# Optimization experiments

Measured on AMD Instinct MI355X. Metric: run time of the kernel, lower is better.

The kernel has to match this reference:

```python
import jax, jax.numpy as jnp
import numpy as np

SUB = 40   # subframe_size
NSUB = 4   # nb_subframes


def _glu(x, w):
    return x * jax.nn.sigmoid(x @ w.T)


def _gru(x, h, w_ih, w_hh):
    # torch.nn.GRUCell (bias=False): gates ordered r, z, n
    H = h.shape[-1]
    gi = x @ w_ih.T
    gh = h @ w_hh.T
    r = jax.nn.sigmoid(gi[:, :H] + gh[:, :H])
    z = jax.nn.sigmoid(gi[:, H:2 * H] + gh[:, H:2 * H])
    n = jnp.tanh(gi[:, 2 * H:] + r * gh[:, 2 * H:])
    return (1.0 - z) * n + z * h


def _fargan_forward(features, period, p):
    B, T, _ = features.shape
    period = jnp.clip(period, 32, 254)

    # ---- FARGANCond ----
    f = features[:, 2:, :]                               # [B, T-2, 20]
    pidx = jnp.clip(period[:, 2:] - 32, 0, 223)
    pe = p['pembed'][pidx]                               # [B, T-2, 12]
    x = jnp.tanh(jnp.concatenate([f, pe], -1) @ p['fd1_w'].T)   # [B, T-2, 64]
    y = jax.lax.conv_general_dilated(
        x.transpose(0, 2, 1), p['fconv1_w'], (1,), 'VALID',
        dimension_numbers=('NCH', 'OIH', 'NCH'))
    y = jnp.tanh(y).transpose(0, 2, 1)                   # [B, T-4, 128]
    cond = jnp.tanh(y @ p['fd2_w'].T)                    # [B, T-4, 320]

    nb_frames = T - 4
    cond_steps = cond.reshape(B, nb_frames, NSUB, 80)
    cond_steps = cond_steps.transpose(1, 2, 0, 3).reshape(nb_frames * NSUB, B, 80)
    pitch = period[:, 3:3 + nb_frames]                   # conv-center aligned pitch
    pitch_steps = jnp.repeat(pitch.T, NSUB, axis=0)      # [steps, B]

    rng = jnp.arange(SUB + 4)

    def step(carry, inp):
        exc_mem, prev_pred, s1, s2, s3, fwc_state = carry
        cond80, per = inp
        gain = 0.2 + 0.8 * jax.nn.sigmoid(cond80 @ p['cg_w'].T + p['cg_b'])
        gain = jnp.clip(gain, 0.001, 20.0)               # [B, 1]
        idx = 256 - per[:, None] + rng[None, :] - 2
        idx = idx - (idx >= 256) * per[:, None]
        idx = jnp.clip(idx, 0, 255)
        pred = jnp.take_along_axis(exc_mem, idx, axis=1) / (1e-5 + gain)  # [B, 44]
        prev = exc_mem[:, -SUB:] / (1e-5 + gain)         # [B, 40]
        tmp = jnp.concatenate([cond80, pred, prev], 1)   # [B, 164]
        fpitch = pred[:, 2:-2]                           # [B, 40]
        xcat = jnp.concatenate([fwc_state, tmp], 1)      # [B, 328]
        fwc_out = _glu(jnp.tanh(xcat @ p['fwc_w'].T), p['fwc_glu_w'])  # [B, 192]
        new_fwc_state = xcat[:, 164:]
        pg = jax.nn.sigmoid(fwc_out @ p['gout_w'].T + p['gout_b'])     # [B, 4]
        s1n = _gru(jnp.concatenate([fwc_out, pg[:, 0:1] * fpitch, prev], 1), s1, p['g1_ih'], p['g1_hh'])
        g1 = _glu(s1n, p['glu1_w'])
        s2n = _gru(jnp.concatenate([g1, pg[:, 1:2] * fpitch, prev], 1), s2, p['g2_ih'], p['g2_hh'])
        g2 = _glu(s2n, p['glu2_w'])
        s3n = _gru(jnp.concatenate([g2, pg[:, 2:3] * fpitch, prev], 1), s3, p['g3_ih'], p['g3_hh'])
        g3 = _glu(s3n, p['glu3_w'])
        skip_in = jnp.concatenate([g1, g2, g3, fwc_out, pg[:, 3:4] * fpitch, prev], 1)  # [B, 688+80]
        skip = _glu(jnp.tanh(skip_in @ p['skip_w'].T), p['skip_glu_w'])
        sig = jnp.tanh(skip @ p['sig_w'].T) * gain       # [B, 40]
        exc_mem = jnp.concatenate([exc_mem[:, SUB:], sig], 1)
        prev_pred = jnp.concatenate([prev_pred[:, SUB:], fpitch], 1)
        return (exc_mem, prev_pred, s1n, s2n, s3n, new_fwc_state), sig

    dt = features.dtype
    carry0 = (jnp.zeros((B, 256), dt), jnp.zeros((B, 256), dt),
              jnp.zeros((B, 160), dt), jnp.zeros((B, 128), dt),
              jnp.zeros((B, 128), dt), jnp.zeros((B, 164), dt))
    _, sigs = jax.lax.scan(jax.checkpoint(step), carry0, (cond_steps, pitch_steps))
    return sigs.transpose(1, 0, 2).reshape(B, -1)        # [B, nb_frames*160]


def _w(key, out_dim, in_dim):
    return jax.random.normal(key, (out_dim, in_dim), jnp.float32) / np.sqrt(in_dim)


def setup_inputs() -> dict:
    key = jax.random.key(0)
    ks = jax.random.split(key, 24)
    B, T = 128, 504
    d = {}
    d['features'] = jax.random.normal(ks[0], (B, T, 20), jnp.float32)
    d['period'] = jax.random.randint(ks[1], (B, T), 32, 255)
    d['pembed'] = jax.random.normal(ks[2], (224, 12), jnp.float32) * 0.3
    d['fd1_w'] = _w(ks[3], 64, 32)
    d['fconv1_w'] = jax.random.normal(ks[4], (128, 64, 3), jnp.float32) / np.sqrt(192.0)
    d['fd2_w'] = _w(ks[5], 320, 128)
    d['cg_w'] = _w(ks[6], 1, 80)
    d['cg_b'] = jnp.zeros((1,), jnp.float32)
    d['fwc_w'] = _w(ks[7], 192, 328)
    d['fwc_glu_w'] = _w(ks[8], 192, 192)
    d['g1_ih'] = _w(ks[9], 480, 272)
    d['g1_hh'] = _w(ks[10], 480, 160)
    d['glu1_w'] = _w(ks[11], 160, 160)
    d['g2_ih'] = _w(ks[12], 384, 240)
    d['g2_hh'] = _w(ks[13], 384, 128)
    d['glu2_w'] = _w(ks[14], 128, 128)
    d['g3_ih'] = _w(ks[15], 384, 208)
    d['g3_hh'] = _w(ks[16], 384, 128)
    d['glu3_w'] = _w(ks[17], 128, 128)
    d['skip_w'] = _w(ks[18], 128, 688)
    d['skip_glu_w'] = _w(ks[19], 128, 128)
    d['sig_w'] = _w(ks[20], 40, 128)
    d['gout_w'] = _w(ks[21], 4, 192)
    d['gout_b'] = jnp.zeros((4,), jnp.float32)
    return d


def reference(features, period, pembed, fd1_w, fconv1_w, fd2_w, cg_w, cg_b,
              fwc_w, fwc_glu_w, g1_ih, g1_hh, glu1_w, g2_ih, g2_hh, glu2_w,
              g3_ih, g3_hh, glu3_w, skip_w, skip_glu_w, sig_w, gout_w, gout_b):
    p = dict(pembed=pembed, fd1_w=fd1_w, fconv1_w=fconv1_w, fd2_w=fd2_w,
             cg_w=cg_w, cg_b=cg_b, fwc_w=fwc_w, fwc_glu_w=fwc_glu_w,
             g1_ih=g1_ih, g1_hh=g1_hh, glu1_w=glu1_w,
             g2_ih=g2_ih, g2_hh=g2_hh, glu2_w=glu2_w,
             g3_ih=g3_ih, g3_hh=g3_hh, glu3_w=glu3_w,
             skip_w=skip_w, skip_glu_w=skip_glu_w, sig_w=sig_w,
             gout_w=gout_w, gout_b=gout_b)
    return _fargan_forward(features, period, p)
```

## Files before the change

kernel.cpp:

```cpp
#include <hip/hip_runtime.h>
#include <hip/hip_fp16.h>
#include <math.h>


#define DEV __device__ __forceinline__

DEV float sigm(float x) { return 1.0f / (1.0f + __expf(-x)); }
DEV float tanh_f(float x) { return 1.0f - 2.0f / (__expf(2.0f * x) + 1.0f); }

typedef _Float16 h2v __attribute__((ext_vector_type(2)));

#if defined(__has_builtin)
#if __has_builtin(__builtin_amdgcn_fdot2)
#define HAVE_FDOT2 1
#endif
#endif

DEV float fdot2(h2v a, h2v b, float c) {
#ifdef HAVE_FDOT2
    return __builtin_amdgcn_fdot2(a, b, c, false);
#else
    return c + (float)a[0] * (float)b[0] + (float)a[1] * (float)b[1];
#endif
}

constexpr size_t STEPS = 2000;
constexpr size_t OFF_X     = 0;
constexpr size_t OFF_Y     = 4200000;
constexpr size_t OFF_GAIN  = 12392000;
constexpr size_t OFF_CONDH = 12648000;
constexpr size_t OFF_W     = 22888000;

constexpr size_t W_FWC     = 0;
constexpr size_t W_FWCGLU  = W_FWC    + 192*352;
constexpr size_t W_GOUT    = W_FWCGLU + 192*192;
constexpr size_t W_G1IH    = W_GOUT   + 4*192;
constexpr size_t W_G1HH    = W_G1IH   + 480*272;
constexpr size_t W_GLU1    = W_G1HH   + 480*160;
constexpr size_t W_G2IH    = W_GLU1   + 160*160;
constexpr size_t W_G2HH    = W_G2IH   + 384*240;
constexpr size_t W_GLU2    = W_G2HH   + 384*128;
constexpr size_t W_G3IH    = W_GLU2   + 128*128;
constexpr size_t W_G3HH    = W_G3IH   + 384*208;
constexpr size_t W_GLU3    = W_G3HH   + 384*128;
constexpr size_t W_SKIP    = W_GLU3   + 128*128;
constexpr size_t W_SKIPGLU = W_SKIP   + 128*704;
constexpr size_t W_SIG     = W_SKIPGLU+ 128*128;

constexpr int WL_FWCGLU = 0;
constexpr int WL_GLU2   = 4608;
constexpr int WL_GLU3   = 6656;
constexpr int WL_TOT    = 8704;

__global__ void k_pack_h(const float* __restrict__ src, __half* __restrict__ dst,
                         int OUT, int K, int KP8) {
    int t = blockIdx.x * 256 + threadIdx.x;
    if (t >= OUT * KP8) return;
    int j = t % OUT;
    int k8 = t / OUT;
    __half* d = dst + (size_t)t * 8;
#pragma unroll
    for (int i = 0; i < 8; ++i) {
        int k = k8 * 8 + i;
        d[i] = (k < K) ? __float2half(src[(size_t)j * K + k]) : __float2half(0.0f);
    }
}

__global__ void k_feat(const float* __restrict__ features, const int* __restrict__ period,
                       const float* __restrict__ pembed, const float* __restrict__ fd1,
                       float* __restrict__ xbuf) {
    int t = blockIdx.x * 256 + threadIdx.x;
    const int total = 128 * 502 * 64;
    if (t >= total) return;
    int o = t & 63;
    int r = t >> 6;
    int ft = r % 502;
    int b = r / 502;
    const float* f = features + ((size_t)b * 504 + ft + 2) * 20;
    int per = period[b * 504 + ft + 2];
    per = min(max(per, 32), 254);
    const float* pe = pembed + (per - 32) * 12;
    const float* w = fd1 + o * 32;
    float acc = 0.0f;
#pragma unroll
    for (int i = 0; i < 20; ++i) acc += f[i] * w[i];
#pragma unroll
    for (int i = 0; i < 12; ++i) acc += pe[i] * w[20 + i];
    xbuf[t] = tanh_f(acc);
}

__global__ void k_conv(const float* __restrict__ xbuf, const float* __restrict__ fconv1,
                       float* __restrict__ ybuf) {
    int t = blockIdx.x * 256 + threadIdx.x;
    const int total = 128 * 500 * 128;
    if (t >= total) return;
    int oc = t & 127;
    int r = t >> 7;
    int tt = r % 500;
    int b = r / 500;
    const float* xp = xbuf + ((size_t)b * 502 + tt) * 64;
    const float* w = fconv1 + oc * 192;
    float acc = 0.0f;
#pragma unroll 8
    for (int i = 0; i < 64; ++i) {
        acc += xp[i] * w[i * 3 + 0];
        acc += xp[64 + i] * w[i * 3 + 1];
        acc += xp[128 + i] * w[i * 3 + 2];
    }
    ybuf[t] = tanh_f(acc);
}

__global__ void k_cond(const float* __restrict__ ybuf, const float* __restrict__ fd2,
                       __half* __restrict__ cond) {
    int b = blockIdx.x / 50;
    int t0 = (blockIdx.x % 50) * 10;
    int tid = threadIdx.x;
    __shared__ float yl[1280];
    for (int i = tid; i < 1280; i += 320)
        yl[i] = ybuf[((size_t)b * 500 + t0) * 128 + i];
    __syncthreads();
    const float* w = fd2 + tid * 128;
    float acc[10];
#pragma unroll
    for (int q = 0; q < 10; ++q) acc[q] = 0.0f;
#pragma unroll 4
    for (int k = 0; k < 128; ++k) {
        float wv = w[k];
#pragma unroll
        for (int q = 0; q < 10; ++q) acc[q] += wv * yl[q * 128 + k];
    }
#pragma unroll
    for (int q = 0; q < 10; ++q)
        cond[((size_t)b * 500 + t0 + q) * 320 + tid] = __float2half(tanh_f(acc[q]));
}

__global__ void k_gain(const __half* __restrict__ cond, const float* __restrict__ cgw,
                       const float* __restrict__ cgb, float* __restrict__ gains) {
    int t = blockIdx.x * 256 + threadIdx.x;
    const int total = 128 * 2000;
    if (t >= total) return;
    int s = t % 2000;
    int b = t / 2000;
    int frame = s >> 2, sub = s & 3;
    const __half* c = cond + ((size_t)b * 500 + frame) * 320 + sub * 80;
    float acc = 0.0f;
#pragma unroll 8
    for (int i = 0; i < 80; ++i) acc += __half2float(c[i]) * cgw[i];
    float g = 0.2f + 0.8f * sigm(acc + cgb[0]);
    g = fminf(20.0f, fmaxf(0.001f, g));
    gains[t] = g;
}

DEV void dot8h(uint4 w, uint4 x, float& a0, float& a1) {
    const h2v* wv = (const h2v*)&w;
    const h2v* xv = (const h2v*)&x;
    a0 = fdot2(wv[0], xv[0], a0);
    a1 = fdot2(wv[1], xv[1], a1);
    a0 = fdot2(wv[2], xv[2], a0);
    a1 = fdot2(wv[3], xv[3], a1);
}

template <int OUT, int KP8, int S>
DEV void mv_partial(const uint4* __restrict__ WT, const __half* __restrict__ x,
                    float* __restrict__ part, int tid) {
    static_assert(KP8 % S == 0, "KP8 % S");
    static_assert(OUT * S <= 1024, "threads");
    constexpr int KS8 = KP8 / S;
    if (tid < OUT * S) {
        int j = tid % OUT;
        int sl = tid / OUT;
        const uint4* w = WT + (size_t)sl * KS8 * OUT + j;
        const uint4* xx = (const uint4*)x + (size_t)sl * KS8;
        float a0 = 0.0f, a1 = 0.0f;
#pragma unroll 4
        for (int k = 0; k < KS8; ++k) dot8h(w[(size_t)k * OUT], xx[k], a0, a1);
        part[tid] = a0 + a1;
    }
}

template <int OUT, int KP8, int S>
DEV void mv_partial_l(const uint4* wl, const __half* __restrict__ x,
                      float* __restrict__ part, int tid) {
    constexpr int KS8 = KP8 / S;
    if (tid < OUT * S) {
        int j = tid % OUT;
        int sl = tid / OUT;
        const uint4* w = wl + (size_t)sl * KS8 * OUT + j;
        const uint4* xx = (const uint4*)x + (size_t)sl * KS8;
        float a0 = 0.0f, a1 = 0.0f;
#pragma unroll
        for (int k = 0; k < KS8; ++k) dot8h(w[(size_t)k * OUT], xx[k], a0, a1);
        part[tid] = a0 + a1;
    }
}

template <int OUT, int KP8A, int KP8B>
DEV void gru_partial(const uint4* __restrict__ wa, const __half* __restrict__ xa,
                     const uint4* __restrict__ wb, const __half* __restrict__ xb,
                     float* __restrict__ pa, float* __restrict__ pb, int tid) {
    static_assert((KP8A % 2 == 0) && (KP8B % 2 == 0), "even");
    constexpr int KA = KP8A / 2, KB = KP8B / 2;
    if (tid < OUT * 2) {
        int j = tid % OUT;
        int sl = tid / OUT;
        {
            const uint4* w = wa + (size_t)sl * KA * OUT + j;
            const uint4* xx = (const uint4*)xa + (size_t)sl * KA;
            float a0 = 0.0f, a1 = 0.0f;
#pragma unroll 4
            for (int k = 0; k < KA; ++k) dot8h(w[(size_t)k * OUT], xx[k], a0, a1);
            pa[tid] = a0 + a1;
        }
        {
            const uint4* w = wb + (size_t)sl * KB * OUT + j;
            const uint4* xx = (const uint4*)xb + (size_t)sl * KB;
            float b0 = 0.0f, b1 = 0.0f;
#pragma unroll 4
            for (int k = 0; k < KB; ++k) dot8h(w[(size_t)k * OUT], xx[k], b0, b1);
            pb[tid] = b0 + b1;
        }
    }
}

template <int H>
DEV void gru_update(const float* __restrict__ pa, const float* __restrict__ pb,
                    float* __restrict__ s, __half* __restrict__ sh, int tid) {
    constexpr int OUT = 3 * H;
    if (tid < H) {
        float gi_r = pa[tid] + pa[OUT + tid];
        float gh_r = pb[tid] + pb[OUT + tid];
        float gi_z = pa[H + tid] + pa[OUT + H + tid];
        float gh_z = pb[H + tid] + pb[OUT + H + tid];
        float gi_n = pa[2 * H + tid] + pa[OUT + 2 * H + tid];
        float gh_n = pb[2 * H + tid] + pb[OUT + 2 * H + tid];
        float r = sigm(gi_r + gh_r);
        float z = sigm(gi_z + gh_z);
        float n = tanh_f(gi_n + r * gh_n);
        float v = (1.0f - z) * n + z * s[tid];
        s[tid] = v;
        sh[tid] = __float2half(v);
    }
}

__global__ __launch_bounds__(1024) void fargan_main(const float* __restrict__ ws,
                                                    const int* __restrict__ period,
                                                    const float* __restrict__ goutb,
                                                    float* __restrict__ out) {
    const int b = blockIdx.x;
    const int tid = threadIdx.x;

    const __half* cond = (const __half*)(ws + OFF_CONDH);
    const float* gains = ws + OFF_GAIN;
    const __half* whb  = (const __half*)(ws + OFF_W);
    const uint4* wFWC     = (const uint4*)(whb + W_FWC);
    const uint4* wFWCGLU  = (const uint4*)(whb + W_FWCGLU);
    const uint4* wGOUT    = (const uint4*)(whb + W_GOUT);
    const uint4* wG1IH    = (const uint4*)(whb + W_G1IH);
    const uint4* wG1HH    = (const uint4*)(whb + W_G1HH);
    const uint4* wGLU1    = (const uint4*)(whb + W_GLU1);
    const uint4* wG2IH    = (const uint4*)(whb + W_G2IH);
    const uint4* wG2HH    = (const uint4*)(whb + W_G2HH);
    const uint4* wGLU2    = (const uint4*)(whb + W_GLU2);
    const uint4* wG3IH    = (const uint4*)(whb + W_G3IH);
    const uint4* wG3HH    = (const uint4*)(whb + W_G3HH);
    const uint4* wGLU3    = (const uint4*)(whb + W_GLU3);
    const uint4* wSKIP    = (const uint4*)(whb + W_SKIP);
    const uint4* wSKIPGLU = (const uint4*)(whb + W_SKIPGLU);
    const uint4* wSIG     = (const uint4*)(whb + W_SIG);

    __shared__ __align__(16) uint4 wlds[WL_TOT];

    __shared__ __align__(16) __half xcat_h[352];
    __shared__ __align__(16) __half inb_h[272];
    __shared__ __align__(16) __half fwcpre_h[192], fwcout_h[192];
    __shared__ __align__(16) __half s1_h[160], s2_h[128], s3_h[128];
    __shared__ __align__(16) __half g1_h[160], g2_h[128], g3_h[128];
    __shared__ __align__(16) __half skipin_h[704], skippre_h[128], skipout_h[128];
    __shared__ __align__(16) float exc[256];
    __shared__ __align__(16) float s1[160], s2[128], s3[128];
    __shared__ __align__(16) float partA[1024], partB[1024];
    __shared__ __align__(16) float fwcpre[192];
    __shared__ __align__(16) float pg[4];
    __shared__ __align__(16) float skippre[128];
    __shared__ __align__(16) float sigraw[40];

    for (int i = tid; i < 4608; i += 1024) wlds[WL_FWCGLU + i] = wFWCGLU[i];
    for (int i = tid; i < 2048; i += 1024) wlds[WL_GLU2 + i] = wGLU2[i];
    for (int i = tid; i < 2048; i += 1024) wlds[WL_GLU3 + i] = wGLU3[i];

    const int j2 = tid % 384;
    const int sl2 = (tid < 768) ? (tid / 384) : 0;
    const uint4* g2b = wG2HH + (size_t)sl2 * 8 * 384 + j2;
    const uint4 c0 = g2b[0 * 384];
    const uint4 c1 = g2b[1 * 384];
    const uint4 c2 = g2b[2 * 384];
    const uint4 c3 = g2b[3 * 384];
    const uint4 c4 = g2b[4 * 384];
    const uint4 c5 = g2b[5 * 384];
    const uint4 c6 = g2b[6 * 384];
    const uint4 c7 = g2b[7 * 384];

    for (int i = tid; i < 256; i += 1024) exc[i] = 0.0f;
    if (tid < 160) { s1[tid] = 0.0f; s1_h[tid] = __float2half(0.0f); }
    if (tid < 128) { s2[tid] = 0.0f; s3[tid] = 0.0f;
                     s2_h[tid] = __float2half(0.0f); s3_h[tid] = __float2half(0.0f); }
    if (tid < 164) xcat_h[tid] = __float2half(0.0f);
    if (tid >= 328 && tid < 352) xcat_h[tid] = __float2half(0.0f);
    if (tid >= 688 && tid < 704) skipin_h[tid] = __float2half(0.0f);
    __syncthreads();

    for (int s = 0; s < (int)STEPS; ++s) {
        const int frame = s >> 2;
        const float gain = gains[(size_t)b * 2000 + s];
        const float ig = 1.0f / (1e-5f + gain);
        int per = period[b * 504 + 3 + frame];
        per = min(max(per, 32), 254);

        if (tid < 80) {
            xcat_h[164 + tid] = cond[((size_t)b * 500 + frame) * 320 + (s & 3) * 80 + tid];
        } else if (tid >= 128 && tid < 172) {
            int j = tid - 128;
            int idx = 254 - per + j;
            if (idx >= 256) idx -= per;
            idx = min(255, max(0, idx));
            xcat_h[244 + j] = __float2half(exc[idx] * ig);
        } else if (tid >= 192 && tid < 232) {
            xcat_h[288 + tid - 192] = __float2half(exc[216 + tid - 192] * ig);
        }
        __syncthreads();

        mv_partial<192, 44, 4>(wFWC, xcat_h, partA, tid);
        __syncthreads();
        if (tid < 192) {
            float a = partA[tid] + partA[192 + tid] + partA[384 + tid] + partA[576 + tid];
            float t = tanh_f(a);
            fwcpre[tid] = t;
            fwcpre_h[tid] = __float2half(t);
        }
        __syncthreads();

        mv_partial_l<192, 24, 4>(wlds + WL_FWCGLU, fwcpre_h, partA, tid);
        if (tid >= 768 && tid < 800) {
            int t2 = tid - 768;
            int j = t2 & 3, sl = t2 >> 2;
            const uint4* w = wGOUT + (sl * 3) * 4 + j;
            const uint4* xx = (const uint4*)fwcpre_h + sl * 3;
            float a0 = 0.0f, a1 = 0.0f;
#pragma unroll
            for (int k = 0; k < 3; ++k) dot8h(w[k * 4], xx[k], a0, a1);
            partB[t2] = a0 + a1;
        } else if (tid >= 832 && tid < 996) {
            xcat_h[tid - 832] = xcat_h[tid - 832 + 164];
        }
        __syncthreads();

        if (tid < 192) {
            float a = partA[tid] + partA[192 + tid] + partA[384 + tid] + partA[576 + tid];
            float v = fwcpre[tid] * sigm(a);
            __half vh = __float2half(v);
            fwcout_h[tid] = vh;
            inb_h[tid] = vh;
        } else if (tid < 232) {
            float a = goutb[0];
#pragma unroll
            for (int sl = 0; sl < 8; ++sl) a += partB[sl * 4];
            inb_h[tid] = __float2half(sigm(a) * __half2float(xcat_h[246 + tid - 192]));
        } else if (tid < 272) {
            inb_h[tid] = xcat_h[288 + tid - 232];
        } else if (tid >= 960 && tid < 964) {
            int j = tid - 960;
            float a = goutb[j];
#pragma unroll
            for (int sl = 0; sl < 8; ++sl) a += partB[sl * 4 + j];
            pg[j] = sigm(a);
        }
        __syncthreads();

        gru_partial<480, 34, 20>(wG1IH, inb_h, wG1HH, s1_h, partA, partB, tid);
        __syncthreads();
        gru_update<160>(partA, partB, s1, s1_h, tid);
        __syncthreads();

        mv_partial<160, 20, 4>(wGLU1, s1_h, partA, tid);
        __syncthreads();
        if (tid < 160) {
            float a = partA[tid] + partA[160 + tid] + partA[320 + tid] + partA[480 + tid];
            float v = s1[tid] * sigm(a);
            __half vh = __float2half(v);
            g1_h[tid] = vh;
            inb_h[tid] = vh;
        } else if (tid < 200) {
            inb_h[tid] = __float2half(pg[1] * __half2float(xcat_h[246 + tid - 160]));
        } else if (tid < 240) {
            inb_h[tid] = xcat_h[288 + tid - 200];
        }
        __syncthreads();

        if (tid < 768) {
            constexpr int KA = 15;
            {
                const uint4* w = wG2IH + (size_t)sl2 * KA * 384 + j2;
                const uint4* xx = (const uint4*)inb_h + (size_t)sl2 * KA;
                float a0 = 0.0f, a1 = 0.0f;
#pragma unroll 4
                for (int k = 0; k < KA; ++k) dot8h(w[(size_t)k * 384], xx[k], a0, a1);
                partA[tid] = a0 + a1;
            }
            {
                const uint4* xb = (const uint4*)s2_h + (size_t)sl2 * 8;
                float b0 = 0.0f, b1 = 0.0f;
                dot8h(c0, xb[0], b0, b1);
                dot8h(c1, xb[1], b0, b1);
                dot8h(c2, xb[2], b0, b1);
                dot8h(c3, xb[3], b0, b1);
                dot8h(c4, xb[4], b0, b1);
                dot8h(c5, xb[5], b0, b1);
                dot8h(c6, xb[6], b0, b1);
                dot8h(c7, xb[7], b0, b1);
                partB[tid] = b0 + b1;
            }
        }
        __syncthreads();
        gru_update<128>(partA, partB, s2, s2_h, tid);
        __syncthreads();

        mv_partial_l<128, 16, 8>(wlds + WL_GLU2, s2_h, partA, tid);
        __syncthreads();
        if (tid < 128) {
            float a = 0.0f;
#pragma unroll
            for (int sl = 0; sl < 8; ++sl) a += partA[sl * 128 + tid];
            float v = s2[tid] * sigm(a);
            __half vh = __float2half(v);
            g2_h[tid] = vh;
            inb_h[tid] = vh;
        } else if (tid < 168) {
            inb_h[tid] = __float2half(pg[2] * __half2float(xcat_h[246 + tid - 128]));
        } else if (tid < 208) {
            inb_h[tid] = xcat_h[288 + tid - 168];
        }
        __syncthreads();

        gru_partial<384, 26, 16>(wG3IH, inb_h, wG3HH, s3_h, partA, partB, tid);
        __syncthreads();
        gru_update<128>(partA, partB, s3, s3_h, tid);
        __syncthreads();

        mv_partial_l<128, 16, 8>(wlds + WL_GLU3, s3_h, partA, tid);
        __syncthreads();
        if (tid < 128) {
            float a = 0.0f;
#pragma unroll
            for (int sl = 0; sl < 8; ++sl) a += partA[sl * 128 + tid];
            float v = s3[tid] * sigm(a);
            __half vh = __float2half(v);
            g3_h[tid] = vh;
            skipin_h[288 + tid] = vh;
        } else if (tid < 288) {
            skipin_h[tid - 128] = g1_h[tid - 128];
        } else if (tid < 416) {
            skipin_h[160 + tid - 288] = g2_h[tid - 288];
        } else if (tid < 608) {
            skipin_h[tid] = fwcout_h[tid - 416];
        } else if (tid < 648) {
            skipin_h[tid] = __float2half(pg[3] * __half2float(xcat_h[246 + tid - 608]));
        } else if (tid < 688) {
            skipin_h[tid] = xcat_h[288 + tid - 648];
        }
        __syncthreads();

        mv_partial<128, 88, 8>(wSKIP, skipin_h, partA, tid);
        __syncthreads();
        if (tid < 128) {
            float a = 0.0f;
#pragma unroll
            for (int sl = 0; sl < 8; ++sl) a += partA[sl * 128 + tid];
            float t = tanh_f(a);
            skippre[tid] = t;
            skippre_h[tid] = __float2half(t);
        }
        __syncthreads();

        mv_partial<128, 16, 8>(wSKIPGLU, skippre_h, partA, tid);
        __syncthreads();
        if (tid < 128) {
            float a = 0.0f;
#pragma unroll
            for (int sl = 0; sl < 8; ++sl) a += partA[sl * 128 + tid];
            skipout_h[tid] = __float2half(skippre[tid] * sigm(a));
        }
        __syncthreads();

        mv_partial<40, 16, 8>(wSIG, skipout_h, partA, tid);
        __syncthreads();
        float keep = (tid < 216) ? exc[tid + 40] : 0.0f;
        if (tid < 40) {
            float a = 0.0f;
#pragma unroll
            for (int sl = 0; sl < 8; ++sl) a += partA[sl * 40 + tid];
            sigraw[tid] = tanh_f(a) * gain;
        }
        __syncthreads();
        if (tid < 216) {
            exc[tid] = keep;
        } else if (tid < 256) {
            float sv = sigraw[tid - 216];
            exc[tid] = sv;
            out[(size_t)b * 80000 + (size_t)s * 40 + (tid - 216)] = sv;
        }
        __syncthreads();
    }
}

extern "C" void kernel_launch(void* const* d_in, const int* in_sizes, int n_in,
                              void* d_out, int out_size, void* d_ws, size_t ws_size,
                              hipStream_t stream) {
    const float* features = (const float*)d_in[0];
    const int*   period   = (const int*)d_in[1];
    const float* pembed   = (const float*)d_in[2];
    const float* fd1_w    = (const float*)d_in[3];
    const float* fconv1_w = (const float*)d_in[4];
    const float* fd2_w    = (const float*)d_in[5];
    const float* cg_w     = (const float*)d_in[6];
    const float* cg_b     = (const float*)d_in[7];
    const float* fwc_w    = (const float*)d_in[8];
    const float* fwc_glu  = (const float*)d_in[9];
    const float* g1_ih    = (const float*)d_in[10];
    const float* g1_hh    = (const float*)d_in[11];
    const float* glu1_w   = (const float*)d_in[12];
    const float* g2_ih    = (const float*)d_in[13];
    const float* g2_hh    = (const float*)d_in[14];
    const float* glu2_w   = (const float*)d_in[15];
    const float* g3_ih    = (const float*)d_in[16];
    const float* g3_hh    = (const float*)d_in[17];
    const float* glu3_w   = (const float*)d_in[18];
    const float* skip_w   = (const float*)d_in[19];
    const float* skip_glu = (const float*)d_in[20];
    const float* sig_w    = (const float*)d_in[21];
    const float* gout_w   = (const float*)d_in[22];
    const float* gout_b   = (const float*)d_in[23];

    float* ws = (float*)d_ws;
    float* out = (float*)d_out;
    __half* wh = (__half*)(ws + OFF_W);

    struct PW { const float* src; size_t off; int out, k, kpad; };
    const PW pws[15] = {
        {fwc_w,    W_FWC,     192, 328, 352}, {fwc_glu, W_FWCGLU, 192, 192, 192},
        {gout_w,   W_GOUT,      4, 192, 192}, {g1_ih,   W_G1IH,   480, 272, 272},
        {g1_hh,    W_G1HH,    480, 160, 160}, {glu1_w,  W_GLU1,   160, 160, 160},
        {g2_ih,    W_G2IH,    384, 240, 240}, {g2_hh,   W_G2HH,   384, 128, 128},
        {glu2_w,   W_GLU2,    128, 128, 128}, {g3_ih,   W_G3IH,   384, 208, 208},
        {g3_hh,    W_G3HH,    384, 128, 128}, {glu3_w,  W_GLU3,   128, 128, 128},
        {skip_w,   W_SKIP,    128, 688, 704}, {skip_glu,W_SKIPGLU,128, 128, 128},
        {sig_w,    W_SIG,      40, 128, 128},
    };
    for (int i = 0; i < 15; ++i) {
        int kp8 = pws[i].kpad / 8;
        int n = pws[i].out * kp8;
        k_pack_h<<<(n + 255) / 256, 256, 0, stream>>>(pws[i].src, wh + pws[i].off,
                                                      pws[i].out, pws[i].k, kp8);
    }

    {
        int n = 128 * 502 * 64;
        k_feat<<<(n + 255) / 256, 256, 0, stream>>>(features, period, pembed, fd1_w,
                                                    ws + OFF_X);
    }
    {
        int n = 128 * 500 * 128;
        k_conv<<<(n + 255) / 256, 256, 0, stream>>>(ws + OFF_X, fconv1_w, ws + OFF_Y);
    }
    k_cond<<<128 * 50, 320, 0, stream>>>(ws + OFF_Y, fd2_w, (__half*)(ws + OFF_CONDH));
    {
        int n = 128 * 2000;
        k_gain<<<(n + 255) / 256, 256, 0, stream>>>((const __half*)(ws + OFF_CONDH),
                                                    cg_w, cg_b, ws + OFF_GAIN);
    }

    fargan_main<<<128, 1024, 0, stream>>>(ws, period, gout_b, out);
}
```

Before: 34.19 ms.

## Process two batch elements per block to reuse each weight load

```diff
diff --git a/kernel.cpp b/kernel.cpp
--- a/kernel.cpp
+++ b/kernel.cpp
@@ -49,8 +49,9 @@
 
 constexpr int WL_FWCGLU = 0;
 constexpr int WL_GLU2   = 4608;
-constexpr int WL_GLU3   = 6656;
-constexpr int WL_TOT    = 8704;
+constexpr int WL_SIG    = 6656;
+constexpr int WL_GOUT   = 7296;
+constexpr int WL_TOT    = 7392;
 
 __global__ void k_pack_h(const float* __restrict__ src, __half* __restrict__ dst,
                          int OUT, int K, int KP8) {
@@ -151,53 +152,64 @@
     gains[t] = g;
 }
 
-DEV void dot8h(uint4 w, uint4 x, float& a0, float& a1) {
+DEV void dot8h2(uint4 w, uint4 x0, uint4 x1,
+                float& a0, float& a1, float& b0, float& b1) {
     const h2v* wv = (const h2v*)&w;
-    const h2v* xv = (const h2v*)&x;
-    a0 = fdot2(wv[0], xv[0], a0);
-    a1 = fdot2(wv[1], xv[1], a1);
-    a0 = fdot2(wv[2], xv[2], a0);
-    a1 = fdot2(wv[3], xv[3], a1);
+    const h2v* x0v = (const h2v*)&x0;
+    const h2v* x1v = (const h2v*)&x1;
+    a0 = fdot2(wv[0], x0v[0], a0);
+    b0 = fdot2(wv[0], x1v[0], b0);
+    a1 = fdot2(wv[1], x0v[1], a1);
+    b1 = fdot2(wv[1], x1v[1], b1);
+    a0 = fdot2(wv[2], x0v[2], a0);
+    b0 = fdot2(wv[2], x1v[2], b0);
+    a1 = fdot2(wv[3], x0v[3], a1);
+    b1 = fdot2(wv[3], x1v[3], b1);
 }
 
 template <int OUT, int KP8, int S>
-DEV void mv_partial(const uint4* __restrict__ WT, const __half* __restrict__ x,
-                    float* __restrict__ part, int tid) {
+DEV void mv2(const uint4* __restrict__ WT, const __half* x0, const __half* x1,
+             float* p0, float* p1, int tid) {
     static_assert(KP8 % S == 0, "KP8 % S");
-    static_assert(OUT * S <= 1024, "threads");
     constexpr int KS8 = KP8 / S;
     if (tid < OUT * S) {
         int j = tid % OUT;
         int sl = tid / OUT;
         const uint4* w = WT + (size_t)sl * KS8 * OUT + j;
-        const uint4* xx = (const uint4*)x + (size_t)sl * KS8;
-        float a0 = 0.0f, a1 = 0.0f;
+        const uint4* xx0 = (const uint4*)x0 + (size_t)sl * KS8;
+        const uint4* xx1 = (const uint4*)x1 + (size_t)sl * KS8;
+        float a0 = 0.0f, a1 = 0.0f, b0 = 0.0f, b1 = 0.0f;
 #pragma unroll 4
-        for (int k = 0; k < KS8; ++k) dot8h(w[(size_t)k * OUT], xx[k], a0, a1);
-        part[tid] = a0 + a1;
+        for (int k = 0; k < KS8; ++k)
+            dot8h2(w[(size_t)k * OUT], xx0[k], xx1[k], a0, a1, b0, b1);
+        p0[tid] = a0 + a1;
+        p1[tid] = b0 + b1;
     }
 }
 
 template <int OUT, int KP8, int S>
-DEV void mv_partial_l(const uint4* wl, const __half* __restrict__ x,
-                      float* __restrict__ part, int tid) {
+DEV void mv2_l(const uint4* wl, const __half* x0, const __half* x1,
+               float* p0, float* p1, int tid) {
     constexpr int KS8 = KP8 / S;
     if (tid < OUT * S) {
         int j = tid % OUT;
         int sl = tid / OUT;
         const uint4* w = wl + (size_t)sl * KS8 * OUT + j;
-        const uint4* xx = (const uint4*)x + (size_t)sl * KS8;
-        float a0 = 0.0f, a1 = 0.0f;
-#pragma unroll
-        for (int k = 0; k < KS8; ++k) dot8h(w[(size_t)k * OUT], xx[k], a0, a1);
-        part[tid] = a0 + a1;
+        const uint4* xx0 = (const uint4*)x0 + (size_t)sl * KS8;
+        const uint4* xx1 = (const uint4*)x1 + (size_t)sl * KS8;
+        float a0 = 0.0f, a1 = 0.0f, b0 = 0.0f, b1 = 0.0f;
+#pragma unroll
+        for (int k = 0; k < KS8; ++k)
+            dot8h2(w[(size_t)k * OUT], xx0[k], xx1[k], a0, a1, b0, b1);
+        p0[tid] = a0 + a1;
+        p1[tid] = b0 + b1;
     }
 }
 
 template <int OUT, int KP8A, int KP8B>
-DEV void gru_partial(const uint4* __restrict__ wa, const __half* __restrict__ xa,
-                     const uint4* __restrict__ wb, const __half* __restrict__ xb,
-                     float* __restrict__ pa, float* __restrict__ pb, int tid) {
+DEV void gru_p2(const uint4* __restrict__ wa, const __half* xa0, const __half* xa1,
+                const uint4* __restrict__ wb, const __half* xb0, const __half* xb1,
+                float* pa0, float* pa1, float* pb0, float* pb1, int tid) {
     static_assert((KP8A % 2 == 0) && (KP8B % 2 == 0), "even");
     constexpr int KA = KP8A / 2, KB = KP8B / 2;
     if (tid < OUT * 2) {
@@ -205,19 +217,25 @@
         int sl = tid / OUT;
         {
             const uint4* w = wa + (size_t)sl * KA * OUT + j;
-            const uint4* xx = (const uint4*)xa + (size_t)sl * KA;
-            float a0 = 0.0f, a1 = 0.0f;
+            const uint4* x0 = (const uint4*)xa0 + (size_t)sl * KA;
+            const uint4* x1 = (const uint4*)xa1 + (size_t)sl * KA;
+            float a0 = 0.0f, a1 = 0.0f, b0 = 0.0f, b1 = 0.0f;
 #pragma unroll 4
-            for (int k = 0; k < KA; ++k) dot8h(w[(size_t)k * OUT], xx[k], a0, a1);
-            pa[tid] = a0 + a1;
+            for (int k = 0; k < KA; ++k)
+                dot8h2(w[(size_t)k * OUT], x0[k], x1[k], a0, a1, b0, b1);
+            pa0[tid] = a0 + a1;
+            pa1[tid] = b0 + b1;
         }
         {
             const uint4* w = wb + (size_t)sl * KB * OUT + j;
-            const uint4* xx = (const uint4*)xb + (size_t)sl * KB;
-            float b0 = 0.0f, b1 = 0.0f;
+            const uint4* x0 = (const uint4*)xb0 + (size_t)sl * KB;
+            const uint4* x1 = (const uint4*)xb1 + (size_t)sl * KB;
+            float a0 = 0.0f, a1 = 0.0f, b0 = 0.0f, b1 = 0.0f;
 #pragma unroll 4
-            for (int k = 0; k < KB; ++k) dot8h(w[(size_t)k * OUT], xx[k], b0, b1);
-            pb[tid] = b0 + b1;
+            for (int k = 0; k < KB; ++k)
+                dot8h2(w[(size_t)k * OUT], x0[k], x1[k], a0, a1, b0, b1);
+            pb0[tid] = a0 + a1;
+            pb1[tid] = b0 + b1;
         }
     }
 }
@@ -246,7 +264,8 @@
                                                     const int* __restrict__ period,
                                                     const float* __restrict__ goutb,
                                                     float* __restrict__ out) {
-    const int b = blockIdx.x;
+    const int bid = blockIdx.x;
+    const int b0 = 2 * bid, b1 = 2 * bid + 1;
     const int tid = threadIdx.x;
 
     const __half* cond = (const __half*)(ws + OFF_CONDH);
@@ -270,243 +289,296 @@
 
     __shared__ __align__(16) uint4 wlds[WL_TOT];
 
-    __shared__ __align__(16) __half xcat_h[352];
-    __shared__ __align__(16) __half inb_h[272];
-    __shared__ __align__(16) __half fwcpre_h[192], fwcout_h[192];
-    __shared__ __align__(16) __half s1_h[160], s2_h[128], s3_h[128];
-    __shared__ __align__(16) __half g1_h[160], g2_h[128], g3_h[128];
-    __shared__ __align__(16) __half skipin_h[704], skippre_h[128], skipout_h[128];
-    __shared__ __align__(16) float exc[256];
-    __shared__ __align__(16) float s1[160], s2[128], s3[128];
-    __shared__ __align__(16) float partA[1024], partB[1024];
-    __shared__ __align__(16) float fwcpre[192];
-    __shared__ __align__(16) float pg[4];
-    __shared__ __align__(16) float skippre[128];
-    __shared__ __align__(16) float sigraw[40];
-
-    for (int i = tid; i < 4608; i += 1024) wlds[WL_FWCGLU + i] = wFWCGLU[i];
-    for (int i = tid; i < 2048; i += 1024) wlds[WL_GLU2 + i] = wGLU2[i];
-    for (int i = tid; i < 2048; i += 1024) wlds[WL_GLU3 + i] = wGLU3[i];
-
-    const int j2 = tid % 384;
-    const int sl2 = (tid < 768) ? (tid / 384) : 0;
-    const uint4* g2b = wG2HH + (size_t)sl2 * 8 * 384 + j2;
-    const uint4 c0 = g2b[0 * 384];
-    const uint4 c1 = g2b[1 * 384];
-    const uint4 c2 = g2b[2 * 384];
-    const uint4 c3 = g2b[3 * 384];
-    const uint4 c4 = g2b[4 * 384];
-    const uint4 c5 = g2b[5 * 384];
-    const uint4 c6 = g2b[6 * 384];
-    const uint4 c7 = g2b[7 * 384];
-
-    for (int i = tid; i < 256; i += 1024) exc[i] = 0.0f;
-    if (tid < 160) { s1[tid] = 0.0f; s1_h[tid] = __float2half(0.0f); }
-    if (tid < 128) { s2[tid] = 0.0f; s3[tid] = 0.0f;
-                     s2_h[tid] = __float2half(0.0f); s3_h[tid] = __float2half(0.0f); }
-    if (tid < 164) xcat_h[tid] = __float2half(0.0f);
-    if (tid >= 328 && tid < 352) xcat_h[tid] = __float2half(0.0f);
-    if (tid >= 688 && tid < 704) skipin_h[tid] = __float2half(0.0f);
+    __shared__ __align__(16) __half xcat_h[2][352];
+    __shared__ __align__(16) __half inb_h[2][272];
+    __shared__ __align__(16) __half fwcpre_h[2][192], fwcout_h[2][192];
+    __shared__ __align__(16) __half s1_h[2][160], s2_h[2][128], s3_h[2][128];
+    __shared__ __align__(16) __half g1_h[2][160], g2_h[2][128], g3_h[2][128];
+    __shared__ __align__(16) __half skipin_h[2][704], skippre_h[2][128], skipout_h[2][128];
+    __shared__ __align__(16) float exc[2][256];
+    __shared__ __align__(16) float s1[2][160], s2[2][128], s3[2][128];
+    __shared__ __align__(16) float partA[2][1024], partB[2][1024];
+    __shared__ __align__(16) float fwcpre[2][192];
+    __shared__ __align__(16) float pg[2][4];
+    __shared__ __align__(16) float skippre[2][128];
+    __shared__ __align__(16) float sigraw[2][40];
+
+    for (int i = tid; i < WL_TOT; i += 1024) {
+        uint4 v;
+        if (i < 4608)      v = wFWCGLU[i];
+        else if (i < 6656) v = wGLU2[i - 4608];
+        else if (i < 7296) v = wSIG[i - 6656];
+        else               v = wGOUT[i - 7296];
+        wlds[i] = v;
+    }
+
+    for (int i = tid; i < 512; i += 1024) ((float*)exc)[i] = 0.0f;
+    if (tid < 160) {
+        s1[0][tid] = 0.0f; s1[1][tid] = 0.0f;
+        s1_h[0][tid] = __float2half(0.0f); s1_h[1][tid] = __float2half(0.0f);
+    }
+    if (tid < 128) {
+        s2[0][tid] = 0.0f; s2[1][tid] = 0.0f;
+        s3[0][tid] = 0.0f; s3[1][tid] = 0.0f;
+        s2_h[0][tid] = __float2half(0.0f); s2_h[1][tid] = __float2half(0.0f);
+        s3_h[0][tid] = __float2half(0.0f); s3_h[1][tid] = __float2half(0.0f);
+    }
+    if (tid < 164) {
+        xcat_h[0][tid] = __float2half(0.0f);
+        xcat_h[1][tid] = __float2half(0.0f);
+    }
+    if (tid >= 328 && tid < 352) {
+        xcat_h[0][tid] = __float2half(0.0f);
+        xcat_h[1][tid] = __float2half(0.0f);
+    }
+    if (tid >= 688 && tid < 704) {
+        skipin_h[0][tid] = __float2half(0.0f);
+        skipin_h[1][tid] = __float2half(0.0f);
+    }
     __syncthreads();
 
     for (int s = 0; s < (int)STEPS; ++s) {
         const int frame = s >> 2;
-        const float gain = gains[(size_t)b * 2000 + s];
-        const float ig = 1.0f / (1e-5f + gain);
-        int per = period[b * 504 + 3 + frame];
-        per = min(max(per, 32), 254);
+        const float gn0 = gains[(size_t)b0 * 2000 + s];
+        const float gn1 = gains[(size_t)b1 * 2000 + s];
+        const float ig0 = 1.0f / (1e-5f + gn0);
+        const float ig1 = 1.0f / (1e-5f + gn1);
+        int per0 = min(max(period[b0 * 504 + 3 + frame], 32), 254);
+        int per1 = min(max(period[b1 * 504 + 3 + frame], 32), 254);
 
         if (tid < 80) {
-            xcat_h[164 + tid] = cond[((size_t)b * 500 + frame) * 320 + (s & 3) * 80 + tid];
+            xcat_h[0][164 + tid] = cond[((size_t)b0 * 500 + frame) * 320 + (s & 3) * 80 + tid];
+            xcat_h[1][164 + tid] = cond[((size_t)b1 * 500 + frame) * 320 + (s & 3) * 80 + tid];
         } else if (tid >= 128 && tid < 172) {
             int j = tid - 128;
-            int idx = 254 - per + j;
-            if (idx >= 256) idx -= per;
-            idx = min(255, max(0, idx));
-            xcat_h[244 + j] = __float2half(exc[idx] * ig);
+            {
+                int idx = 254 - per0 + j;
+                if (idx >= 256) idx -= per0;
+                idx = min(255, max(0, idx));
+                xcat_h[0][244 + j] = __float2half(exc[0][idx] * ig0);
+            }
+            {
+                int idx = 254 - per1 + j;
+                if (idx >= 256) idx -= per1;
+                idx = min(255, max(0, idx));
+                xcat_h[1][244 + j] = __float2half(exc[1][idx] * ig1);
+            }
         } else if (tid >= 192 && tid < 232) {
-            xcat_h[288 + tid - 192] = __float2half(exc[216 + tid - 192] * ig);
-        }
-        __syncthreads();
-
-        mv_partial<192, 44, 4>(wFWC, xcat_h, partA, tid);
+            int j = tid - 192;
+            xcat_h[0][288 + j] = __float2half(exc[0][216 + j] * ig0);
+            xcat_h[1][288 + j] = __float2half(exc[1][216 + j] * ig1);
+        }
+        __syncthreads();
+
+        mv2<192, 44, 4>(wFWC, xcat_h[0], xcat_h[1], partA[0], partA[1], tid);
         __syncthreads();
         if (tid < 192) {
-            float a = partA[tid] + partA[192 + tid] + partA[384 + tid] + partA[576 + tid];
-            float t = tanh_f(a);
-            fwcpre[tid] = t;
-            fwcpre_h[tid] = __float2half(t);
-        }
-        __syncthreads();
-
-        mv_partial_l<192, 24, 4>(wlds + WL_FWCGLU, fwcpre_h, partA, tid);
+#pragma unroll
+            for (int g = 0; g < 2; ++g) {
+                float a = partA[g][tid] + partA[g][192 + tid] + partA[g][384 + tid] + partA[g][576 + tid];
+                float t = tanh_f(a);
+                fwcpre[g][tid] = t;
+                fwcpre_h[g][tid] = __float2half(t);
+            }
+        }
+        __syncthreads();
+
+        mv2_l<192, 24, 4>(wlds + WL_FWCGLU, fwcpre_h[0], fwcpre_h[1], partA[0], partA[1], tid);
         if (tid >= 768 && tid < 800) {
             int t2 = tid - 768;
             int j = t2 & 3, sl = t2 >> 2;
-            const uint4* w = wGOUT + (sl * 3) * 4 + j;
-            const uint4* xx = (const uint4*)fwcpre_h + sl * 3;
-            float a0 = 0.0f, a1 = 0.0f;
-#pragma unroll
-            for (int k = 0; k < 3; ++k) dot8h(w[k * 4], xx[k], a0, a1);
-            partB[t2] = a0 + a1;
+            const uint4* w = wlds + WL_GOUT + (sl * 3) * 4 + j;
+            const uint4* xx0 = (const uint4*)fwcpre_h[0] + sl * 3;
+            const uint4* xx1 = (const uint4*)fwcpre_h[1] + sl * 3;
+            float a0 = 0.0f, a1 = 0.0f, c0 = 0.0f, c1 = 0.0f;
+#pragma unroll
+            for (int k = 0; k < 3; ++k) dot8h2(w[k * 4], xx0[k], xx1[k], a0, a1, c0, c1);
+            partB[0][t2] = a0 + a1;
+            partB[1][t2] = c0 + c1;
         } else if (tid >= 832 && tid < 996) {
-            xcat_h[tid - 832] = xcat_h[tid - 832 + 164];
+            xcat_h[0][tid - 832] = xcat_h[0][tid - 832 + 164];
+            xcat_h[1][tid - 832] = xcat_h[1][tid - 832 + 164];
         }
         __syncthreads();
 
         if (tid < 192) {
-            float a = partA[tid] + partA[192 + tid] + partA[384 + tid] + partA[576 + tid];
-            float v = fwcpre[tid] * sigm(a);
-            __half vh = __float2half(v);
-            fwcout_h[tid] = vh;
-            inb_h[tid] = vh;
+#pragma unroll
+            for (int g = 0; g < 2; ++g) {
+                float a = partA[g][tid] + partA[g][192 + tid] + partA[g][384 + tid] + partA[g][576 + tid];
+                float v = fwcpre[g][tid] * sigm(a);
+                __half vh = __float2half(v);
+                fwcout_h[g][tid] = vh;
+                inb_h[g][tid] = vh;
+            }
         } else if (tid < 232) {
-            float a = goutb[0];
-#pragma unroll
-            for (int sl = 0; sl < 8; ++sl) a += partB[sl * 4];
-            inb_h[tid] = __float2half(sigm(a) * __half2float(xcat_h[246 + tid - 192]));
+#pragma unroll
+            for (int g = 0; g < 2; ++g) {
+                float a = goutb[0];
+#pragma unroll
+                for (int sl = 0; sl < 8; ++sl) a += partB[g][sl * 4];
+                inb_h[g][tid] = __float2half(sigm(a) * __half2float(xcat_h[g][246 + tid - 192]));
+            }
         } else if (tid < 272) {
-            inb_h[tid] = xcat_h[288 + tid - 232];
+            inb_h[0][tid] = xcat_h[0][288 + tid - 232];
+            inb_h[1][tid] = xcat_h[1][288 + tid - 232];
         } else if (tid >= 960 && tid < 964) {
             int j = tid - 960;
-            float a = goutb[j];
-#pragma unroll
-            for (int sl = 0; sl < 8; ++sl) a += partB[sl * 4 + j];
-            pg[j] = sigm(a);
-        }
-        __syncthreads();
-
-        gru_partial<480, 34, 20>(wG1IH, inb_h, wG1HH, s1_h, partA, partB, tid);
-        __syncthreads();
-        gru_update<160>(partA, partB, s1, s1_h, tid);
-        __syncthreads();
-
-        mv_partial<160, 20, 4>(wGLU1, s1_h, partA, tid);
+#pragma unroll
+            for (int g = 0; g < 2; ++g) {
+                float a = goutb[j];
+#pragma unroll
+                for (int sl = 0; sl < 8; ++sl) a += partB[g][sl * 4 + j];
+                pg[g][j] = sigm(a);
+            }
+        }
+        __syncthreads();
+
+        gru_p2<480, 34, 20>(wG1IH, inb_h[0], inb_h[1], wG1HH, s1_h[0], s1_h[1],
+                            partA[0], partA[1], partB[0], partB[1], tid);
+        __syncthreads();
+        gru_update<160>(partA[0], partB[0], s1[0], s1_h[0], tid);
+        gru_update<160>(partA[1], partB[1], s1[1], s1_h[1], tid);
+        __syncthreads();
+
+        mv2<160, 20, 4>(wGLU1, s1_h[0], s1_h[1], partA[0], partA[1], tid);
         __syncthreads();
         if (tid < 160) {
-            float a = partA[tid] + partA[160 + tid] + partA[320 + tid] + partA[480 + tid];
-            float v = s1[tid] * sigm(a);
-            __half vh = __float2half(v);
-            g1_h[tid] = vh;
-            inb_h[tid] = vh;
+#pragma unroll
+            for (int g = 0; g < 2; ++g) {
+                float a = partA[g][tid] + partA[g][160 + tid] + partA[g][320 + tid] + partA[g][480 + tid];
+                float v = s1[g][tid] * sigm(a);
+                __half vh = __float2half(v);
+                g1_h[g][tid] = vh;
+                inb_h[g][tid] = vh;
+            }
         } else if (tid < 200) {
-            inb_h[tid] = __float2half(pg[1] * __half2float(xcat_h[246 + tid - 160]));
+            inb_h[0][tid] = __float2half(pg[0][1] * __half2float(xcat_h[0][246 + tid - 160]));
+            inb_h[1][tid] = __float2half(pg[1][1] * __half2float(xcat_h[1][246 + tid - 160]));
         } else if (tid < 240) {
-            inb_h[tid] = xcat_h[288 + tid - 200];
-        }
-        __syncthreads();
-
-        if (tid < 768) {
-            constexpr int KA = 15;
-            {
-                const uint4* w = wG2IH + (size_t)sl2 * KA * 384 + j2;
-                const uint4* xx = (const uint4*)inb_h + (size_t)sl2 * KA;
-                float a0 = 0.0f, a1 = 0.0f;
-#pragma unroll 4
-                for (int k = 0; k < KA; ++k) dot8h(w[(size_t)k * 384], xx[k], a0, a1);
-                partA[tid] = a0 + a1;
-            }
-            {
-                const uint4* xb = (const uint4*)s2_h + (size_t)sl2 * 8;
-                float b0 = 0.0f, b1 = 0.0f;
-                dot8h(c0, xb[0], b0, b1);
-                dot8h(c1, xb[1], b0, b1);
-                dot8h(c2, xb[2], b0, b1);
-                dot8h(c3, xb[3], b0, b1);
-                dot8h(c4, xb[4], b0, b1);
-                dot8h(c5, xb[5], b0, b1);
-                dot8h(c6, xb[6], b0, b1);
-                dot8h(c7, xb[7], b0, b1);
-                partB[tid] = b0 + b1;
-            }
-        }
-        __syncthreads();
-        gru_update<128>(partA, partB, s2, s2_h, tid);
-        __syncthreads();
-
-        mv_partial_l<128, 16, 8>(wlds + WL_GLU2, s2_h, partA, tid);
+            inb_h[0][tid] = xcat_h[0][288 + tid - 200];
+            inb_h[1][tid] = xcat_h[1][288 + tid - 200];
+        }
+        __syncthreads();
+
+        gru_p2<384, 30, 16>(wG2IH, inb_h[0], inb_h[1], wG2HH, s2_h[0], s2_h[1],
+                            partA[0], partA[1], partB[0], partB[1], tid);
+        __syncthreads();
+        gru_update<128>(partA[0], partB[0], s2[0], s2_h[0], tid);
+        gru_update<128>(partA[1], partB[1], s2[1], s2_h[1], tid);
+        __syncthreads();
+
+        mv2_l<128, 16, 8>(wlds + WL_GLU2, s2_h[0], s2_h[1], partA[0], partA[1], tid);
         __syncthreads();
         if (tid < 128) {
-            float a = 0.0f;
-#pragma unroll
-            for (int sl = 0; sl < 8; ++sl) a += partA[sl * 128 + tid];
-            float v = s2[tid] * sigm(a);
-            __half vh = __float2half(v);
-            g2_h[tid] = vh;
-            inb_h[tid] = vh;
+#pragma unroll
+            for (int g = 0; g < 2; ++g) {
+                float a = 0.0f;
+#pragma unroll
+                for (int sl = 0; sl < 8; ++sl) a += partA[g][sl * 128 + tid];
+                float v = s2[g][tid] * sigm(a);
+                __half vh = __float2half(v);
+                g2_h[g][tid] = vh;
+                inb_h[g][tid] = vh;
+            }
         } else if (tid < 168) {
-            inb_h[tid] = __float2half(pg[2] * __half2float(xcat_h[246 + tid - 128]));
+            inb_h[0][tid] = __float2half(pg[0][2] * __half2float(xcat_h[0][246 + tid - 128]));
+            inb_h[1][tid] = __float2half(pg[1][2] * __half2float(xcat_h[1][246 + tid - 128]));
         } else if (tid < 208) {
-            inb_h[tid] = xcat_h[288 + tid - 168];
-        }
-        __syncthreads();
-
-        gru_partial<384, 26, 16>(wG3IH, inb_h, wG3HH, s3_h, partA, partB, tid);
-        __syncthreads();
-        gru_update<128>(partA, partB, s3, s3_h, tid);
-        __syncthreads();
-
-        mv_partial_l<128, 16, 8>(wlds + WL_GLU3, s3_h, partA, tid);
+            inb_h[0][tid] = xcat_h[0][288 + tid - 168];
+            inb_h[1][tid] = xcat_h[1][288 + tid - 168];
+        }
+        __syncthreads();
+
+        gru_p2<384, 26, 16>(wG3IH, inb_h[0], inb_h[1], wG3HH, s3_h[0], s3_h[1],
+                            partA[0], partA[1], partB[0], partB[1], tid);
+        __syncthreads();
+        gru_update<128>(partA[0], partB[0], s3[0], s3_h[0], tid);
+        gru_update<128>(partA[1], partB[1], s3[1], s3_h[1], tid);
+        __syncthreads();
+
+        mv2<128, 16, 8>(wGLU3, s3_h[0], s3_h[1], partA[0], partA[1], tid);
         __syncthreads();
         if (tid < 128) {
-            float a = 0.0f;
-#pragma unroll
-            for (int sl = 0; sl < 8; ++sl) a += partA[sl * 128 + tid];
-            float v = s3[tid] * sigm(a);
-            __half vh = __float2half(v);
-            g3_h[tid] = vh;
-            skipin_h[288 + tid] = vh;
+#pragma unroll
+            for (int g = 0; g < 2; ++g) {
+                float a = 0.0f;
+#pragma unroll
+                for (int sl = 0; sl < 8; ++sl) a += partA[g][sl * 128 + tid];
+                float v = s3[g][tid] * sigm(a);
+                __half vh = __float2half(v);
+                g3_h[g][tid] = vh;
+                skipin_h[g][288 + tid] = vh;
+            }
         } else if (tid < 288) {
-            skipin_h[tid - 128] = g1_h[tid - 128];
+            skipin_h[0][tid - 128] = g1_h[0][tid - 128];
+            skipin_h[1][tid - 128] = g1_h[1][tid - 128];
         } else if (tid < 416) {
-            skipin_h[160 + tid - 288] = g2_h[tid - 288];
+            skipin_h[0][160 + tid - 288] = g2_h[0][tid - 288];
+            skipin_h[1][160 + tid - 288] = g2_h[1][tid - 288];
         } else if (tid < 608) {
-            skipin_h[tid] = fwcout_h[tid - 416];
+            skipin_h[0][tid] = fwcout_h[0][tid - 416];
+            skipin_h[1][tid] = fwcout_h[1][tid - 416];
         } else if (tid < 648) {
-            skipin_h[tid] = __float2half(pg[3] * __half2float(xcat_h[246 + tid - 608]));
+            skipin_h[0][tid] = __float2half(pg[0][3] * __half2float(xcat_h[0][246 + tid - 608]));
+            skipin_h[1][tid] = __float2half(pg[1][3] * __half2float(xcat_h[1][246 + tid - 608]));
         } else if (tid < 688) {
-            skipin_h[tid] = xcat_h[288 + tid - 648];
-        }
-        __syncthreads();
-
-        mv_partial<128, 88, 8>(wSKIP, skipin_h, partA, tid);
+            skipin_h[0][tid] = xcat_h[0][288 + tid - 648];
+            skipin_h[1][tid] = xcat_h[1][288 + tid - 648];
+        }
+        __syncthreads();
+
+        mv2<128, 88, 8>(wSKIP, skipin_h[0], skipin_h[1], partA[0], partA[1], tid);
         __syncthreads();
         if (tid < 128) {
-            float a = 0.0f;
-#pragma unroll
-            for (int sl = 0; sl < 8; ++sl) a += partA[sl * 128 + tid];
-            float t = tanh_f(a);
-            skippre[tid] = t;
-            skippre_h[tid] = __float2half(t);
-        }
-        __syncthreads();
-
-        mv_partial<128, 16, 8>(wSKIPGLU, skippre_h, partA, tid);
+#pragma unroll
+            for (int g = 0; g < 2; ++g) {
+                float a = 0.0f;
+#pragma unroll
+                for (int sl = 0; sl < 8; ++sl) a += partA[g][sl * 128 + tid];
+                float t = tanh_f(a);
+                skippre[g][tid] = t;
+                skippre_h[g][tid] = __float2half(t);
+            }
+        }
+        __syncthreads();
+
+        mv2<128, 16, 8>(wSKIPGLU, skippre_h[0], skippre_h[1], partA[0], partA[1], tid);
         __syncthreads();
         if (tid < 128) {
-            float a = 0.0f;
-#pragma unroll
-            for (int sl = 0; sl < 8; ++sl) a += partA[sl * 128 + tid];
-            skipout_h[tid] = __float2half(skippre[tid] * sigm(a));
-        }
-        __syncthreads();
-
-        mv_partial<40, 16, 8>(wSIG, skipout_h, partA, tid);
-        __syncthreads();
-        float keep = (tid < 216) ? exc[tid + 40] : 0.0f;
+#pragma unroll
+            for (int g = 0; g < 2; ++g) {
+                float a = 0.0f;
+#pragma unroll
+                for (int sl = 0; sl < 8; ++sl) a += partA[g][sl * 128 + tid];
+                skipout_h[g][tid] = __float2half(skippre[g][tid] * sigm(a));
+            }
+        }
+        __syncthreads();
+
+        mv2_l<40, 16, 8>(wlds + WL_SIG, skipout_h[0], skipout_h[1], partA[0], partA[1], tid);
+        __syncthreads();
+        float keep0 = (tid < 216) ? exc[0][tid + 40] : 0.0f;
+        float keep1 = (tid < 216) ? exc[1][tid + 40] : 0.0f;
         if (tid < 40) {
-            float a = 0.0f;
-#pragma unroll
-            for (int sl = 0; sl < 8; ++sl) a += partA[sl * 40 + tid];
-            sigraw[tid] = tanh_f(a) * gain;
+#pragma unroll
+            for (int g = 0; g < 2; ++g) {
+                float a = 0.0f;
+#pragma unroll
+                for (int sl = 0; sl < 8; ++sl) a += partA[g][sl * 40 + tid];
+                sigraw[g][tid] = tanh_f(a) * (g == 0 ? gn0 : gn1);
+            }
         }
         __syncthreads();
         if (tid < 216) {
-            exc[tid] = keep;
+            exc[0][tid] = keep0;
+            exc[1][tid] = keep1;
         } else if (tid < 256) {
-            float sv = sigraw[tid - 216];
-            exc[tid] = sv;
-            out[(size_t)b * 80000 + (size_t)s * 40 + (tid - 216)] = sv;
+            float sv0 = sigraw[0][tid - 216];
+            float sv1 = sigraw[1][tid - 216];
+            exc[0][tid] = sv0;
+            exc[1][tid] = sv1;
+            out[(size_t)b0 * 80000 + (size_t)s * 40 + (tid - 216)] = sv0;
+            out[(size_t)b1 * 80000 + (size_t)s * 40 + (tid - 216)] = sv1;
         }
         __syncthreads();
     }
@@ -578,5 +650,5 @@
                                                     cg_w, cg_b, ws + OFF_GAIN);
     }
 
-    fargan_main<<<128, 1024, 0, stream>>>(ws, period, gout_b, out);
-}
+    fargan_main<<<64, 1024, 0, stream>>>(ws, period, gout_b, out);
+}
```

New measurement: 42.80 ms. 1.25x slower.
